# Optimization experiments

Measured on AMD Instinct MI355X. Metric: run time of the kernel, lower is better.

## Reference

```python
import jax, jax.numpy as jnp
import numpy as np

KH = KW = 5          # deformable kernel (matches offset_channels = 2*5*5)
PAD = 2              # (5-1)//2
DG = 4               # deformable groups


def conv3d(x, w, padding, bias=None):
    # x: [N,C,D,H,W], w: [O,I,kd,kh,kw]
    out = jax.lax.conv_general_dilated(
        x, w, window_strides=(1, 1, 1), padding=padding,
        dimension_numbers=('NCDHW', 'OIDHW', 'NCDHW'))
    if bias is not None:
        out = out + bias[None, :, None, None, None]
    return out


def deform_conv2d(x, offset, weight, pad=PAD, dg=DG):
    """torchvision/mmcv-style deformable conv, stride 1, groups=1, no bias.
    x: [N,C,H,W]; offset: [N, dg*2*K, H, W] ordered (group, k, (dy,dx));
    weight: [Cout, C, KH, KW]."""
    N, C, H, W = x.shape
    K = KH * KW
    off = offset.reshape(N, dg, K, 2, H, W)
    ky, kx = jnp.meshgrid(jnp.arange(KH), jnp.arange(KW), indexing='ij')
    ky = ky.reshape(K).astype(x.dtype)
    kx = kx.reshape(K).astype(x.dtype)
    # absolute sampling positions: [N,dg,K,H,W]
    base_y = ky[:, None, None] - pad + jnp.arange(H, dtype=x.dtype)[None, :, None]
    base_x = kx[:, None, None] - pad + jnp.arange(W, dtype=x.dtype)[None, None, :]
    sy = base_y[None, None] + off[:, :, :, 0]
    sx = base_x[None, None] + off[:, :, :, 1]
    y0 = jnp.floor(sy)
    x0 = jnp.floor(sx)
    wy = sy - y0
    wx = sx - x0
    y0i = y0.astype(jnp.int32)
    x0i = x0.astype(jnp.int32)
    Cg = C // dg
    xg = x.reshape(N, dg, Cg, H * W)

    def gather(yi, xi):
        valid = (yi >= 0) & (yi < H) & (xi >= 0) & (xi < W)
        yc = jnp.clip(yi, 0, H - 1)
        xc = jnp.clip(xi, 0, W - 1)
        idx = (yc * W + xc).reshape(N, dg, 1, K * H * W)
        v = jnp.take_along_axis(xg, idx, axis=3).reshape(N, dg, Cg, K, H, W)
        return v * valid[:, :, None].astype(x.dtype)

    v00 = gather(y0i, x0i)
    v01 = gather(y0i, x0i + 1)
    v10 = gather(y0i + 1, x0i)
    v11 = gather(y0i + 1, x0i + 1)
    wy_ = wy[:, :, None]
    wx_ = wx[:, :, None]
    samp = (v00 * (1 - wy_) * (1 - wx_) + v01 * (1 - wy_) * wx_
            + v10 * wy_ * (1 - wx_) + v11 * wy_ * wx_)
    samp = samp.reshape(N, C, K, H, W)             # deform groups only affect offsets
    wmat = weight.reshape(weight.shape[0], C, K)
    return jnp.einsum('nckhw,ock->nohw', samp, wmat)


def setup_inputs() -> dict:
    key = jax.random.key(0)
    k0, k1, k2, k3, k4 = jax.random.split(key, 5)
    bs, C, T, H, W = 1, 256, 4, 48, 48
    x = jax.random.normal(k0, (bs, C, T, H, W), dtype=jnp.float32)
    # spatio_offset: Conv3d(C -> dg*2*K, kernel (1,5,5), pad (0,2,2), no bias)
    w_off = jax.random.normal(k1, (DG * 2 * KH * KW, C, 1, KH, KW), dtype=jnp.float32) * 0.01
    # spatio_adaption: DeformConv2d weight, init std=0.01 (per init_weights)
    w_def = jax.random.normal(k2, (C, C, KH, KW), dtype=jnp.float32) * 0.01
    # temporal: Conv3d(C -> C, kernel (3,3,3), pad (1,1,1), with bias)
    fan_in = C * 27
    w_temp = jax.random.normal(k3, (C, C, 3, 3, 3), dtype=jnp.float32) * (1.0 / np.sqrt(fan_in))
    b_temp = jax.random.normal(k4, (C,), dtype=jnp.float32) * 0.01
    return {'x': x, 'w_off': w_off, 'w_def': w_def, 'w_temp': w_temp, 'b_temp': b_temp}


def reference(x, w_off, w_def, w_temp, b_temp):
    bs, C, T, H, W = x.shape
    # offset branch uses detached input (torch: x.detach())
    offset = conv3d(jax.lax.stop_gradient(x), w_off, [(0, 0), (PAD, PAD), (PAD, PAD)])
    off_fold = offset.transpose(0, 2, 1, 3, 4).reshape(bs * T, -1, H, W)
    x_fold = x.transpose(0, 2, 1, 3, 4).reshape(bs * T, C, H, W)
    x_spatio_fold = deform_conv2d(x_fold, off_fold, w_def)
    x_spatio = x_spatio_fold.reshape(bs, T, C, H, W).transpose(0, 2, 1, 3, 4)
    # cascaded=False branch: temporal conv on original x, then residual sum
    x_temporal = conv3d(x, w_temp, [(1, 1), (1, 1), (1, 1)], b_temp)
    return x_spatio + x_temporal
```

## Files before the change

kernel.cpp:

```cpp
#include <hip/hip_runtime.h>
#include <hip/hip_bf16.h>

#define T    4
#define C    256
#define H    48
#define W    48
#define HW   2304
#define OFFC 200
#define CK5  6400
#define CK9  2304
#define NFULL 9216
#define BPAD 72

typedef __attribute__((ext_vector_type(8))) short bf16x8;
typedef __attribute__((ext_vector_type(4))) float f32x4;

__device__ __forceinline__ unsigned short f2bf(float f) {
    unsigned int u = __float_as_uint(f);
    return (unsigned short)((u + 0x7FFFu + ((u >> 16) & 1u)) >> 16);
}
__device__ __forceinline__ float bflo(unsigned int v) { return __uint_as_float(v << 16); }
__device__ __forceinline__ float bfhi(unsigned int v) { return __uint_as_float(v & 0xFFFF0000u); }
__device__ __forceinline__ unsigned int pack2(float lo, float hi) {
    __hip_bfloat162 h = __float22bfloat162_rn(make_float2(lo, hi));
    return *reinterpret_cast<unsigned int*>(&h);
}
__device__ __forceinline__ void gload16(const void* g, void* l) {
    __builtin_amdgcn_global_load_lds(
        (const __attribute__((address_space(1))) unsigned int*)g,
        (__attribute__((address_space(3))) unsigned int*)l, 16, 0, 0);
}

__global__ __launch_bounds__(256) void prep_xt_k(const float* __restrict__ x,
                                                 const float* __restrict__ w_off,
                                                 const float* __restrict__ w_def,
                                                 const float* __restrict__ w_temp,
                                                 const float* __restrict__ bias,
                                                 unsigned short* __restrict__ wbo,
                                                 unsigned short* __restrict__ wbd,
                                                 unsigned short* __restrict__ wbT,
                                                 float* __restrict__ offb,
                                                 float* __restrict__ out,
                                                 unsigned short* __restrict__ xt) {
    __shared__ float tile[64][65];
    if (blockIdx.x >= 24320) {
        const int zb = blockIdx.x - 24320;
        const int p0 = (zb % 36) * 64, c0 = ((zb / 36) & 3) * 64, t = zb / 144;
        const int px = threadIdx.x & 63, sub = threadIdx.x >> 6;
        for (int cl = sub; cl < 64; cl += 4)
            tile[px][cl] = x[((long)(c0 + cl) * T + t) * HW + p0 + px];
        __syncthreads();
        const int seg = sub * 16;
        unsigned int pk[8];
        #pragma unroll
        for (int d = 0; d < 8; ++d)
            pk[d] = pack2(tile[px][seg + d * 2], tile[px][seg + d * 2 + 1]);
        unsigned short* orow = xt + ((long)t * HW + p0 + px) * 256 + c0 + seg;
        *(uint4*)(orow + 0) = make_uint4(pk[0], pk[1], pk[2], pk[3]);
        *(uint4*)(orow + 8) = make_uint4(pk[4], pk[5], pk[6], pk[7]);
        return;
    }
    long i = (long)blockIdx.x * 256 + threadIdx.x;
    if (i < 1638400) {
        const int c = (int)(i & 255); const int rest = (int)(i >> 8);
        const int q = rest % 25, o = rest / 25;
        wbo[(long)o * CK5 + q * 256 + c] =
            (o < OFFC) ? f2bf(w_off[((long)o * 256 + c) * 25 + q]) : (unsigned short)0;
    } else if (i < 3276800) {
        i -= 1638400;
        const int c = (int)(i & 255); const int rest = (int)(i >> 8);
        const int q = rest % 25, o = rest / 25;
        wbd[(long)o * CK5 + q * 256 + c] = f2bf(w_def[((long)o * 256 + c) * 25 + q]);
    } else if (i < 5046272) {
        i -= 3276800;
        const int c = (int)(i & 255); const int rest = (int)(i >> 8);
        const int j = rest % 9, oo = rest / 9;
        const int o = oo & 255, kt = oo >> 8;
        wbT[(long)kt * (256 * CK9) + (long)o * CK9 + j * 256 + c] =
            f2bf(w_temp[((long)o * 256 + c) * 27 + kt * 9 + j]);
    } else if (i < 5636096) {
        i -= 5046272;
        ((float4*)offb)[i] = make_float4(0.f, 0.f, 0.f, 0.f);
    } else {
        i -= 5636096;
        const float b = bias[(int)(i / 2304)];
        ((float4*)out)[i] = make_float4(b, b, b, b);
    }
}

__device__ __forceinline__ void mfma_iter(const unsigned short* __restrict__ Asl,
                                          const unsigned short* __restrict__ Bsl,
                                          int wave, int quad, int l16, f32x4 acc[4][2]) {
    const int wm = (wave & 1) * 64, wn = (wave >> 1) * 32;
    #pragma unroll
    for (int kh = 0; kh < 2; ++kh) {
        bf16x8 af[4], bfr[2];
        #pragma unroll
        for (int i = 0; i < 4; ++i) {
            const int row = wm + i * 16 + l16;
            const int slot = (kh * 4 + quad + (l16 & 7)) & 7;
            af[i] = *(const bf16x8*)(Asl + row * 64 + slot * 8);
        }
        #pragma unroll
        for (int j = 0; j < 2; ++j)
            bfr[j] = *(const bf16x8*)(Bsl + (wn + j * 16 + l16) * BPAD + kh * 32 + quad * 8);
        #pragma unroll
        for (int i = 0; i < 4; ++i)
            #pragma unroll
            for (int j = 0; j < 2; ++j)
                acc[i][j] = __builtin_amdgcn_mfma_f32_16x16x32_bf16(af[i], bfr[j], acc[i][j], 0, 0, 0);
    }
}
__device__ __forceinline__ void epilogue_atomic(float* __restrict__ Cf, int m0, int n0,
                                                int wave, int quad, int l16,
                                                int Mvalid, f32x4 acc[4][2]) {
    const int wm = (wave & 1) * 64, wn = (wave >> 1) * 32;
    #pragma unroll
    for (int i = 0; i < 4; ++i)
        #pragma unroll
        for (int rr = 0; rr < 4; ++rr) {
            const int o = m0 + wm + i * 16 + quad * 4 + rr;
            if (o >= Mvalid) continue;
            #pragma unroll
            for (int j = 0; j < 2; ++j)
                unsafeAtomicAdd(Cf + (long)o * NFULL + n0 + wn + j * 16 + l16, acc[i][j][rr]);
        }
}

__global__ __launch_bounds__(256, 4) void gemm_off_k(const unsigned short* __restrict__ A,
                                                     const unsigned short* __restrict__ xt,
                                                     float* __restrict__ Cf) {
    __shared__ unsigned short Asl[128 * 64];
    __shared__ unsigned short Bsl[128 * BPAD];
    const int tid = threadIdx.x;
    const int wave = tid >> 6, lane = tid & 63;
    const int quad = lane >> 4, l16 = lane & 15;
    const int n0 = blockIdx.x * 128, m0 = blockIdx.y * 128, k0 = blockIdx.z * 1280;
    const int t = n0 / HW, p0 = n0 - t * HW;
    const int wm = (wave & 1) * 64, wn = (wave >> 1) * 64;

    const int r8 = lane >> 3, s8 = lane & 7;
    const int qg = (s8 - r8) & 7;
    const long ldAb = (long)CK5 * 2;
    const char* Ap = (const char*)A + (long)(m0 + wave * 32 + r8) * ldAb
                     + (long)k0 * 2 + qg * 16;
    const long rstep8 = 8 * ldAb;
    unsigned short* la = Asl + wave * 2048;

    const int px = tid >> 1, half = tid & 1;
    const int p = p0 + px, h = p / 48, w = p - h * 48;
    const unsigned short* xts = xt + (long)t * HW * 256 + half * 32;

    auto produce = [&](int kk, uint4 v[4]) {
        const int q = kk >> 8, cb = kk & 255;
        const int d = q / 5;
        const int y = h + d - 2, xx = w + (q - d * 5) - 2;
        v[0] = make_uint4(0u, 0u, 0u, 0u); v[1] = v[0]; v[2] = v[0]; v[3] = v[0];
        if ((y >= 0) & (y < 48) & (xx >= 0) & (xx < 48)) {
            const unsigned short* bp = xts + (y * 48 + xx) * 256 + cb;
            #pragma unroll
            for (int d4 = 0; d4 < 4; ++d4) v[d4] = *(const uint4*)(bp + d4 * 8);
        }
    };

    uint4 cv[4];
    produce(k0, cv);

    f32x4 acc[4][4] = {};
    for (int i = 0; i < 20; ++i) {
        __syncthreads();
        #pragma unroll
        for (int c2 = 0; c2 < 4; ++c2) gload16(Ap + c2 * rstep8, la + c2 * 512);
        Ap += 128;
        #pragma unroll
        for (int d4 = 0; d4 < 4; ++d4)
            *(uint4*)(Bsl + px * BPAD + half * 32 + d4 * 8) = cv[d4];
        __syncthreads();
        if (i + 1 < 20) produce(k0 + (i + 1) * 64, cv);
        #pragma unroll
        for (int kh = 0; kh < 2; ++kh) {
            bf16x8 af[4], bfr[4];
            #pragma unroll
            for (int ii = 0; ii < 4; ++ii) {
                const int row = wm + ii * 16 + l16;
                const int slot = (kh * 4 + quad + (l16 & 7)) & 7;
                af[ii] = *(const bf16x8*)(Asl + row * 64 + slot * 8);
            }
            #pragma unroll
            for (int j = 0; j < 4; ++j)
                bfr[j] = *(const bf16x8*)(Bsl + (wn + j * 16 + l16) * BPAD + kh * 32 + quad * 8);
            #pragma unroll
            for (int ii = 0; ii < 4; ++ii)
                #pragma unroll
                for (int j = 0; j < 4; ++j)
                    acc[ii][j] = __builtin_amdgcn_mfma_f32_16x16x32_bf16(af[ii], bfr[j], acc[ii][j], 0, 0, 0);
        }
    }
    #pragma unroll
    for (int i = 0; i < 4; ++i)
        #pragma unroll
        for (int rr = 0; rr < 4; ++rr) {
            const int o = m0 + wm + i * 16 + quad * 4 + rr;
            if (o >= OFFC) continue;
            #pragma unroll
            for (int j = 0; j < 4; ++j)
                unsafeAtomicAdd(Cf + (long)o * NFULL + n0 + wn + j * 16 + l16, acc[i][j][rr]);
        }
}

__device__ __forceinline__ void pos_calc(int h, int w, int q, float dy, float dx,
                                         float wgt[4], int idx[4]) {
    const int d = q / 5;
    const int qy = d - 2, qx = q - d * 5 - 2;
    const float sy = (float)(h + qy) + dy;
    const float sx = (float)(w + qx) + dx;
    const float y0f = floorf(sy), x0f = floorf(sx);
    const float wy = sy - y0f, wx = sx - x0f;
    const int y0 = (int)y0f, x0 = (int)x0f;
    const int y1 = y0 + 1, x1 = x0 + 1;
    float w00 = (1.f - wy) * (1.f - wx);
    float w01 = (1.f - wy) * wx;
    float w10 = wy * (1.f - wx);
    float w11 = wy * wx;
    const bool vy0 = (y0 >= 0) & (y0 < 48), vy1 = (y1 >= 0) & (y1 < 48);
    const bool vx0 = (x0 >= 0) & (x0 < 48), vx1 = (x1 >= 0) & (x1 < 48);
    if (!(vy0 & vx0)) w00 = 0.f;
    if (!(vy0 & vx1)) w01 = 0.f;
    if (!(vy1 & vx0)) w10 = 0.f;
    if (!(vy1 & vx1)) w11 = 0.f;
    const int yc0 = min(max(y0, 0), 47), yc1 = min(max(y1, 0), 47);
    const int xc0 = min(max(x0, 0), 47), xc1 = min(max(x1, 0), 47);
    wgt[0] = w00; wgt[1] = w01; wgt[2] = w10; wgt[3] = w11;
    idx[0] = yc0 * 48 + xc0; idx[1] = yc0 * 48 + xc1;
    idx[2] = yc1 * 48 + xc0; idx[3] = yc1 * 48 + xc1;
}
__device__ __forceinline__ uint4 blend4(const uint4 u[4], const float wgt[4]) {
    unsigned int pk[4];
    #pragma unroll
    for (int qi = 0; qi < 4; ++qi) {
        const unsigned int a = ((const unsigned int*)&u[0])[qi];
        const unsigned int b = ((const unsigned int*)&u[1])[qi];
        const unsigned int c = ((const unsigned int*)&u[2])[qi];
        const unsigned int d = ((const unsigned int*)&u[3])[qi];
        const float rl = wgt[0] * bflo(a) + wgt[1] * bflo(b) + wgt[2] * bflo(c) + wgt[3] * bflo(d);
        const float rh = wgt[0] * bfhi(a) + wgt[1] * bfhi(b) + wgt[2] * bfhi(c) + wgt[3] * bfhi(d);
        pk[qi] = pack2(rl, rh);
    }
    return make_uint4(pk[0], pk[1], pk[2], pk[3]);
}

__device__ __forceinline__ void gemm_def_body(unsigned short* __restrict__ Asl,
                                              unsigned short* __restrict__ Bsl,
                                              const unsigned short* __restrict__ A,
                                              const unsigned short* __restrict__ xt,
                                              const float* __restrict__ offb,
                                              float* __restrict__ Cf,
                                              int m0, int n0, int k0) {
    const int tid = threadIdx.x;
    const int wave = tid >> 6, lane = tid & 63;
    const int quad = lane >> 4, l16 = lane & 15;
    const int t = n0 / HW, p0 = n0 - t * HW;
    const int px = tid >> 2, seg = tid & 3;
    const int p = p0 + px, h = p / 48, w = p - h * 48;
    const int nabs = n0 + px;
    const unsigned short* xts = xt + (long)t * HW * 256 + seg * 8;

    const int r8 = lane >> 3, s8 = lane & 7;
    const int qg = (s8 - r8) & 7;
    const long ldAb = (long)CK5 * 2;
    const char* Ap = (const char*)A + (long)(m0 + wave * 32 + r8) * ldAb
                     + (long)k0 * 2 + qg * 16;
    const long rstep8 = 8 * ldAb;
    unsigned short* la = Asl + wave * 2048;

    auto off_load = [&](int kk, float& dy, float& dx) {
        const int q = kk >> 8, g = (kk & 255) >> 6;
        dy = offb[(long)(g * 50 + 2 * q) * NFULL + nabs];
        dx = offb[(long)(g * 50 + 2 * q + 1) * NFULL + nabs];
    };
    auto corners = [&](int kk, float dy, float dx, uint4 u[8], float wgt[4]) {
        const int cb = kk & 255;
        int idx[4];
        pos_calc(h, w, kk >> 8, dy, dx, wgt, idx);
        #pragma unroll
        for (int cn = 0; cn < 4; ++cn) {
            const unsigned short* bp = xts + idx[cn] * 256 + cb;
            u[cn]     = *(const uint4*)bp;
            u[cn + 4] = *(const uint4*)(bp + 32);
        }
    };

    uint4 pkv0, pkv1;
    float dyN, dxN;
    {
        float dy0, dx0;
        off_load(k0, dy0, dx0);
        uint4 u[8]; float wg[4];
        corners(k0, dy0, dx0, u, wg);
        pkv0 = blend4(u, wg);
        pkv1 = blend4(u + 4, wg);
        off_load(k0 + 64, dyN, dxN);
    }

    f32x4 acc[4][2] = {};
    for (int i = 0; i < 25; ++i) {
        const int kk = k0 + i * 64;
        __syncthreads();
        #pragma unroll
        for (int c2 = 0; c2 < 4; ++c2) gload16(Ap + c2 * rstep8, la + c2 * 512);
        Ap += 128;
        *(uint4*)(Bsl + px * BPAD + seg * 8)      = pkv0;
        *(uint4*)(Bsl + px * BPAD + 32 + seg * 8) = pkv1;
        __syncthreads();
        const bool more = (i + 1 < 25);
        uint4 u[8]; float wg[4];
        if (more) {
            corners(kk + 64, dyN, dxN, u, wg);
            if (i + 2 < 25) off_load(kk + 128, dyN, dxN);
        }
        mfma_iter(Asl, Bsl, wave, quad, l16, acc);
        if (more) {
            pkv0 = blend4(u, wg);
            pkv1 = blend4(u + 4, wg);
        }
    }
    epilogue_atomic(Cf, m0, n0, wave, quad, l16, C, acc);
}

__device__ __forceinline__ void gemm_temp_body(unsigned short* __restrict__ Asl,
                                               unsigned short* __restrict__ Bsl,
                                               const unsigned short* __restrict__ A,
                                               const unsigned short* __restrict__ xt, int tsrc,
                                               float* __restrict__ Cf,
                                               int m0, int n0, int k0) {
    const int tid = threadIdx.x;
    const int wave = tid >> 6, lane = tid & 63;
    const int quad = lane >> 4, l16 = lane & 15;
    const int t = n0 / HW, p0 = n0 - t * HW;
    const int px = tid >> 2, seg = tid & 3;
    const int p = p0 + px, h = p / 48, w = p - h * 48;
    const unsigned short* xts = xt + (long)tsrc * HW * 256 + seg * 8;

    const int r8 = lane >> 3, s8 = lane & 7;
    const int qg = (s8 - r8) & 7;
    const long ldAb = (long)CK9 * 2;
    const char* Ap = (const char*)A + (long)(m0 + wave * 32 + r8) * ldAb
                     + (long)k0 * 2 + qg * 16;
    const long rstep8 = 8 * ldAb;
    unsigned short* la = Asl + wave * 2048;

    auto produce = [&](int kk, uint4& v0, uint4& v1) {
        const int q = kk >> 8, cb = kk & 255;
        const int d = q / 3;
        const int y = h + d - 1, xx = w + (q - d * 3) - 1;
        v0 = make_uint4(0u, 0u, 0u, 0u); v1 = v0;
        if ((y >= 0) & (y < 48) & (xx >= 0) & (xx < 48)) {
            const unsigned short* bp = xts + (y * 48 + xx) * 256 + cb;
            v0 = *(const uint4*)bp; v1 = *(const uint4*)(bp + 32);
        }
    };

    uint4 cv0, cv1;
    produce(k0, cv0, cv1);

    f32x4 acc[4][2] = {};
    for (int i = 0; i < 18; ++i) {
        __syncthreads();
        #pragma unroll
        for (int c2 = 0; c2 < 4; ++c2) gload16(Ap + c2 * rstep8, la + c2 * 512);
        Ap += 128;
        *(uint4*)(Bsl + px * BPAD + seg * 8)      = cv0;
        *(uint4*)(Bsl + px * BPAD + 32 + seg * 8) = cv1;
        __syncthreads();
        if (i + 1 < 18) produce(k0 + (i + 1) * 64, cv0, cv1);
        mfma_iter(Asl, Bsl, wave, quad, l16, acc);
    }
    epilogue_atomic(Cf, m0, n0, wave, quad, l16, C, acc);
}

__global__ __launch_bounds__(256, 4) void gemm_dt_k(const unsigned short* __restrict__ wbd,
                                                    const unsigned short* __restrict__ wbT,
                                                    const unsigned short* __restrict__ xt,
                                                    const float* __restrict__ offb,
                                                    float* __restrict__ out) {
    __shared__ unsigned short Asl[128 * 64];
    __shared__ unsigned short Bsl[64 * BPAD];
    const int z = blockIdx.z, n0 = blockIdx.x * 64, m0 = blockIdx.y * 128;
    if (z < 4) {
        gemm_def_body(Asl, Bsl, wbd, xt, offb, out, m0, n0, z * 1600);
    } else {
        const int zz = z - 4, kt = zz >> 1, half = zz & 1;
        const int t = n0 / HW, tsrc = t + kt - 1;
        if (tsrc < 0 || tsrc >= T) return;
        gemm_temp_body(Asl, Bsl, wbT + (long)kt * 256 * CK9, xt, tsrc, out,
                       m0, n0, half * 1152);
    }
}

extern "C" void kernel_launch(void* const* d_in, const int* in_sizes, int n_in,
                              void* d_out, int out_size, void* d_ws, size_t ws_size,
                              hipStream_t stream) {
    const float* x      = (const float*)d_in[0];
    const float* w_off  = (const float*)d_in[1];
    const float* w_def  = (const float*)d_in[2];
    const float* w_temp = (const float*)d_in[3];
    const float* b_temp = (const float*)d_in[4];
    float* out = (float*)d_out;

    unsigned short* xt   = (unsigned short*)d_ws;
    float*          offb = (float*)((char*)d_ws + 4718592ul);
    unsigned short* wbo  = (unsigned short*)((char*)d_ws + 14155776ul);
    unsigned short* wbd  = (unsigned short*)((char*)d_ws + 17432576ul);
    unsigned short* wbT  = (unsigned short*)((char*)d_ws + 20709376ul);

    prep_xt_k<<<24896, 256, 0, stream>>>(x, w_off, w_def, w_temp, b_temp,
                                         wbo, wbd, wbT, offb, out, xt);
    gemm_off_k<<<dim3(72, 2, 5), 256, 0, stream>>>(wbo, xt, offb);
    gemm_dt_k<<<dim3(144, 2, 10), 256, 0, stream>>>(wbd, wbT, xt, offb, out);
}
```

Measured before the change: 289.3 us.

## Double K-tile depth to 128 in deform/temporal GEMMs and rebalance split-K

The fused deformable and temporal GEMM kernel now stages 128-wide K tiles instead of 64, using a new swizzled A-staging helper and a wider padded B tile. This halves the number of barrier-separated iterations, and each thread gathers and blends 32 channels per bilinear sample instead of 16. Split-K is rebalanced: the deform part goes from 4 to 5 chunks, the temporal part drops its 2-way K split, and the offset GEMM goes from 5 to 10 K-splits. The larger shared-memory footprint forces launch bounds down to 3 blocks per SM. Per-thread register pressure for the 16 corner vectors also rises.

```diff
diff --git a/kernel.cpp b/kernel.cpp
--- a/kernel.cpp
+++ b/kernel.cpp
@@ -10,7 +10,8 @@
 #define CK5  6400
 #define CK9  2304
 #define NFULL 9216
-#define BPAD 72
+#define BPAD64  72
+#define BPAD128 136
 
 typedef __attribute__((ext_vector_type(8))) short bf16x8;
 typedef __attribute__((ext_vector_type(4))) float f32x4;
@@ -88,54 +89,15 @@
     }
 }
 
-__device__ __forceinline__ void mfma_iter(const unsigned short* __restrict__ Asl,
-                                          const unsigned short* __restrict__ Bsl,
-                                          int wave, int quad, int l16, f32x4 acc[4][2]) {
-    const int wm = (wave & 1) * 64, wn = (wave >> 1) * 32;
-    #pragma unroll
-    for (int kh = 0; kh < 2; ++kh) {
-        bf16x8 af[4], bfr[2];
-        #pragma unroll
-        for (int i = 0; i < 4; ++i) {
-            const int row = wm + i * 16 + l16;
-            const int slot = (kh * 4 + quad + (l16 & 7)) & 7;
-            af[i] = *(const bf16x8*)(Asl + row * 64 + slot * 8);
-        }
-        #pragma unroll
-        for (int j = 0; j < 2; ++j)
-            bfr[j] = *(const bf16x8*)(Bsl + (wn + j * 16 + l16) * BPAD + kh * 32 + quad * 8);
-        #pragma unroll
-        for (int i = 0; i < 4; ++i)
-            #pragma unroll
-            for (int j = 0; j < 2; ++j)
-                acc[i][j] = __builtin_amdgcn_mfma_f32_16x16x32_bf16(af[i], bfr[j], acc[i][j], 0, 0, 0);
-    }
-}
-__device__ __forceinline__ void epilogue_atomic(float* __restrict__ Cf, int m0, int n0,
-                                                int wave, int quad, int l16,
-                                                int Mvalid, f32x4 acc[4][2]) {
-    const int wm = (wave & 1) * 64, wn = (wave >> 1) * 32;
-    #pragma unroll
-    for (int i = 0; i < 4; ++i)
-        #pragma unroll
-        for (int rr = 0; rr < 4; ++rr) {
-            const int o = m0 + wm + i * 16 + quad * 4 + rr;
-            if (o >= Mvalid) continue;
-            #pragma unroll
-            for (int j = 0; j < 2; ++j)
-                unsafeAtomicAdd(Cf + (long)o * NFULL + n0 + wn + j * 16 + l16, acc[i][j][rr]);
-        }
-}
-
 __global__ __launch_bounds__(256, 4) void gemm_off_k(const unsigned short* __restrict__ A,
                                                      const unsigned short* __restrict__ xt,
                                                      float* __restrict__ Cf) {
     __shared__ unsigned short Asl[128 * 64];
-    __shared__ unsigned short Bsl[128 * BPAD];
+    __shared__ unsigned short Bsl[128 * BPAD64];
     const int tid = threadIdx.x;
     const int wave = tid >> 6, lane = tid & 63;
     const int quad = lane >> 4, l16 = lane & 15;
-    const int n0 = blockIdx.x * 128, m0 = blockIdx.y * 128, k0 = blockIdx.z * 1280;
+    const int n0 = blockIdx.x * 128, m0 = blockIdx.y * 128, k0 = blockIdx.z * 640;
     const int t = n0 / HW, p0 = n0 - t * HW;
     const int wm = (wave & 1) * 64, wn = (wave >> 1) * 64;
 
@@ -167,16 +129,16 @@
     produce(k0, cv);
 
     f32x4 acc[4][4] = {};
-    for (int i = 0; i < 20; ++i) {
+    for (int i = 0; i < 10; ++i) {
         __syncthreads();
         #pragma unroll
         for (int c2 = 0; c2 < 4; ++c2) gload16(Ap + c2 * rstep8, la + c2 * 512);
         Ap += 128;
         #pragma unroll
         for (int d4 = 0; d4 < 4; ++d4)
-            *(uint4*)(Bsl + px * BPAD + half * 32 + d4 * 8) = cv[d4];
-        __syncthreads();
-        if (i + 1 < 20) produce(k0 + (i + 1) * 64, cv);
+            *(uint4*)(Bsl + px * BPAD64 + half * 32 + d4 * 8) = cv[d4];
+        __syncthreads();
+        if (i + 1 < 10) produce(k0 + (i + 1) * 64, cv);
         #pragma unroll
         for (int kh = 0; kh < 2; ++kh) {
             bf16x8 af[4], bfr[4];
@@ -188,7 +150,7 @@
             }
             #pragma unroll
             for (int j = 0; j < 4; ++j)
-                bfr[j] = *(const bf16x8*)(Bsl + (wn + j * 16 + l16) * BPAD + kh * 32 + quad * 8);
+                bfr[j] = *(const bf16x8*)(Bsl + (wn + j * 16 + l16) * BPAD64 + kh * 32 + quad * 8);
             #pragma unroll
             for (int ii = 0; ii < 4; ++ii)
                 #pragma unroll
@@ -206,6 +168,76 @@
             for (int j = 0; j < 4; ++j)
                 unsafeAtomicAdd(Cf + (long)o * NFULL + n0 + wn + j * 16 + l16, acc[i][j][rr]);
         }
+}
+
+__device__ __forceinline__ void mfma_iter128(const unsigned short* __restrict__ Asl,
+                                             const unsigned short* __restrict__ Bsl,
+                                             int wave, int quad, int l16, f32x4 acc[4][2]) {
+    const int wm = (wave & 1) * 64, wn = (wave >> 1) * 32;
+    #pragma unroll
+    for (int kh = 0; kh < 4; ++kh) {
+        const int kc = kh * 4 + quad;
+        bf16x8 af[4], bfr[2];
+        #pragma unroll
+        for (int i = 0; i < 4; ++i) {
+            const int row = wm + i * 16 + l16;
+            const int slot = (((kc & 7) + (l16 & 7)) & 7) | (kc & 8);
+            af[i] = *(const bf16x8*)(Asl + row * 128 + slot * 8);
+        }
+        #pragma unroll
+        for (int j = 0; j < 2; ++j)
+            bfr[j] = *(const bf16x8*)(Bsl + (wn + j * 16 + l16) * BPAD128 + kh * 32 + quad * 8);
+        #pragma unroll
+        for (int i = 0; i < 4; ++i)
+            #pragma unroll
+            for (int j = 0; j < 2; ++j)
+                acc[i][j] = __builtin_amdgcn_mfma_f32_16x16x32_bf16(af[i], bfr[j], acc[i][j], 0, 0, 0);
+    }
+}
+__device__ __forceinline__ void epilogue_atomic(float* __restrict__ Cf, int m0, int n0,
+                                                int wave, int quad, int l16,
+                                                int Mvalid, f32x4 acc[4][2]) {
+    const int wm = (wave & 1) * 64, wn = (wave >> 1) * 32;
+    #pragma unroll
+    for (int i = 0; i < 4; ++i)
+        #pragma unroll
+        for (int rr = 0; rr < 4; ++rr) {
+            const int o = m0 + wm + i * 16 + quad * 4 + rr;
+            if (o >= Mvalid) continue;
+            #pragma unroll
+            for (int j = 0; j < 2; ++j)
+                unsafeAtomicAdd(Cf + (long)o * NFULL + n0 + wn + j * 16 + l16, acc[i][j][rr]);
+        }
+}
+
+struct AStage128 {
+    const char* Ap0;
+    const char* Ap1;
+    long rstep;
+    unsigned short* la;
+};
+__device__ __forceinline__ AStage128 astage_init(const unsigned short* A, long ldA,
+                                                 int m0, int k0, int wave, int lane,
+                                                 unsigned short* Asl) {
+    const int r4 = lane >> 4, s8 = lane & 7, hi8 = lane & 8;
+    const int row0 = r4, row1 = 4 + r4;
+    const int g0 = ((s8 - row0) & 7) | hi8;
+    const int g1 = ((s8 - row1) & 7) | hi8;
+    AStage128 st;
+    const long ldAb = ldA * 2;
+    st.Ap0 = (const char*)A + (long)(m0 + wave * 32 + row0) * ldAb + (long)k0 * 2 + g0 * 16;
+    st.Ap1 = (const char*)A + (long)(m0 + wave * 32 + row1) * ldAb + (long)k0 * 2 + g1 * 16;
+    st.rstep = 8 * ldAb;
+    st.la = Asl + wave * 32 * 128;
+    return st;
+}
+__device__ __forceinline__ void astage_issue(AStage128& st) {
+    #pragma unroll
+    for (int pr = 0; pr < 4; ++pr) {
+        gload16(st.Ap0 + pr * st.rstep, st.la + (2 * pr) * 512);
+        gload16(st.Ap1 + pr * st.rstep, st.la + (2 * pr + 1) * 512);
+    }
+    st.Ap0 += 256; st.Ap1 += 256;
 }
 
 __device__ __forceinline__ void pos_calc(int h, int w, int q, float dy, float dx,
@@ -234,14 +266,16 @@
     idx[0] = yc0 * 48 + xc0; idx[1] = yc0 * 48 + xc1;
     idx[2] = yc1 * 48 + xc0; idx[3] = yc1 * 48 + xc1;
 }
-__device__ __forceinline__ uint4 blend4(const uint4 u[4], const float wgt[4]) {
+__device__ __forceinline__ uint4 blend1(const uint4& ua, const uint4& ub,
+                                        const uint4& uc, const uint4& ud,
+                                        const float wgt[4]) {
     unsigned int pk[4];
     #pragma unroll
     for (int qi = 0; qi < 4; ++qi) {
-        const unsigned int a = ((const unsigned int*)&u[0])[qi];
-        const unsigned int b = ((const unsigned int*)&u[1])[qi];
-        const unsigned int c = ((const unsigned int*)&u[2])[qi];
-        const unsigned int d = ((const unsigned int*)&u[3])[qi];
+        const unsigned int a = ((const unsigned int*)&ua)[qi];
+        const unsigned int b = ((const unsigned int*)&ub)[qi];
+        const unsigned int c = ((const unsigned int*)&uc)[qi];
+        const unsigned int d = ((const unsigned int*)&ud)[qi];
         const float rl = wgt[0] * bflo(a) + wgt[1] * bflo(b) + wgt[2] * bflo(c) + wgt[3] * bflo(d);
         const float rh = wgt[0] * bfhi(a) + wgt[1] * bfhi(b) + wgt[2] * bfhi(c) + wgt[3] * bfhi(d);
         pk[qi] = pack2(rl, rh);
@@ -263,66 +297,61 @@
     const int px = tid >> 2, seg = tid & 3;
     const int p = p0 + px, h = p / 48, w = p - h * 48;
     const int nabs = n0 + px;
-    const unsigned short* xts = xt + (long)t * HW * 256 + seg * 8;
-
-    const int r8 = lane >> 3, s8 = lane & 7;
-    const int qg = (s8 - r8) & 7;
-    const long ldAb = (long)CK5 * 2;
-    const char* Ap = (const char*)A + (long)(m0 + wave * 32 + r8) * ldAb
-                     + (long)k0 * 2 + qg * 16;
-    const long rstep8 = 8 * ldAb;
-    unsigned short* la = Asl + wave * 2048;
+    const unsigned short* xts = xt + (long)t * HW * 256 + seg * 32;
+
+    AStage128 st = astage_init(A, CK5, m0, k0, wave, lane, Asl);
 
     auto off_load = [&](int kk, float& dy, float& dx) {
-        const int q = kk >> 8, g = (kk & 255) >> 6;
+        const int q = kk >> 8;
+        const int g = ((kk & 255) >> 6) + (seg >> 1);
         dy = offb[(long)(g * 50 + 2 * q) * NFULL + nabs];
         dx = offb[(long)(g * 50 + 2 * q + 1) * NFULL + nabs];
     };
-    auto corners = [&](int kk, float dy, float dx, uint4 u[8], float wgt[4]) {
+    auto corners = [&](int kk, float dy, float dx, uint4 u[16], float wgt[4]) {
         const int cb = kk & 255;
         int idx[4];
         pos_calc(h, w, kk >> 8, dy, dx, wgt, idx);
         #pragma unroll
         for (int cn = 0; cn < 4; ++cn) {
             const unsigned short* bp = xts + idx[cn] * 256 + cb;
-            u[cn]     = *(const uint4*)bp;
-            u[cn + 4] = *(const uint4*)(bp + 32);
+            #pragma unroll
+            for (int d4 = 0; d4 < 4; ++d4) u[cn * 4 + d4] = *(const uint4*)(bp + d4 * 8);
         }
     };
-
-    uint4 pkv0, pkv1;
+    auto blend_all = [&](const uint4 u[16], const float wg[4], uint4 pk[4]) {
+        #pragma unroll
+        for (int d4 = 0; d4 < 4; ++d4)
+            pk[d4] = blend1(u[d4], u[4 + d4], u[8 + d4], u[12 + d4], wg);
+    };
+
+    uint4 pk[4];
     float dyN, dxN;
     {
         float dy0, dx0;
         off_load(k0, dy0, dx0);
-        uint4 u[8]; float wg[4];
+        uint4 u[16]; float wg[4];
         corners(k0, dy0, dx0, u, wg);
-        pkv0 = blend4(u, wg);
-        pkv1 = blend4(u + 4, wg);
-        off_load(k0 + 64, dyN, dxN);
+        blend_all(u, wg, pk);
+        off_load(k0 + 128, dyN, dxN);
     }
 
     f32x4 acc[4][2] = {};
-    for (int i = 0; i < 25; ++i) {
-        const int kk = k0 + i * 64;
-        __syncthreads();
-        #pragma unroll
-        for (int c2 = 0; c2 < 4; ++c2) gload16(Ap + c2 * rstep8, la + c2 * 512);
-        Ap += 128;
-        *(uint4*)(Bsl + px * BPAD + seg * 8)      = pkv0;
-        *(uint4*)(Bsl + px * BPAD + 32 + seg * 8) = pkv1;
-        __syncthreads();
-        const bool more = (i + 1 < 25);
-        uint4 u[8]; float wg[4];
+    for (int i = 0; i < 10; ++i) {
+        const int kk = k0 + i * 128;
+        __syncthreads();
+        astage_issue(st);
+        #pragma unroll
+        for (int d4 = 0; d4 < 4; ++d4)
+            *(uint4*)(Bsl + px * BPAD128 + seg * 32 + d4 * 8) = pk[d4];
+        __syncthreads();
+        const bool more = (i + 1 < 10);
+        uint4 u[16]; float wg[4];
         if (more) {
-            corners(kk + 64, dyN, dxN, u, wg);
-            if (i + 2 < 25) off_load(kk + 128, dyN, dxN);
-        }
-        mfma_iter(Asl, Bsl, wave, quad, l16, acc);
-        if (more) {
-            pkv0 = blend4(u, wg);
-            pkv1 = blend4(u + 4, wg);
-        }
+            corners(kk + 128, dyN, dxN, u, wg);
+            if (i + 2 < 10) off_load(kk + 256, dyN, dxN);
+        }
+        mfma_iter128(Asl, Bsl, wave, quad, l16, acc);
+        if (more) blend_all(u, wg, pk);
     }
     epilogue_atomic(Cf, m0, n0, wave, quad, l16, C, acc);
 }
@@ -332,68 +361,61 @@
                                                const unsigned short* __restrict__ A,
                                                const unsigned short* __restrict__ xt, int tsrc,
                                                float* __restrict__ Cf,
-                                               int m0, int n0, int k0) {
+                                               int m0, int n0) {
     const int tid = threadIdx.x;
     const int wave = tid >> 6, lane = tid & 63;
     const int quad = lane >> 4, l16 = lane & 15;
     const int t = n0 / HW, p0 = n0 - t * HW;
     const int px = tid >> 2, seg = tid & 3;
     const int p = p0 + px, h = p / 48, w = p - h * 48;
-    const unsigned short* xts = xt + (long)tsrc * HW * 256 + seg * 8;
-
-    const int r8 = lane >> 3, s8 = lane & 7;
-    const int qg = (s8 - r8) & 7;
-    const long ldAb = (long)CK9 * 2;
-    const char* Ap = (const char*)A + (long)(m0 + wave * 32 + r8) * ldAb
-                     + (long)k0 * 2 + qg * 16;
-    const long rstep8 = 8 * ldAb;
-    unsigned short* la = Asl + wave * 2048;
-
-    auto produce = [&](int kk, uint4& v0, uint4& v1) {
+    const unsigned short* xts = xt + (long)tsrc * HW * 256 + seg * 32;
+
+    AStage128 st = astage_init(A, CK9, m0, 0, wave, lane, Asl);
+
+    auto produce = [&](int kk, uint4 v[4]) {
         const int q = kk >> 8, cb = kk & 255;
         const int d = q / 3;
         const int y = h + d - 1, xx = w + (q - d * 3) - 1;
-        v0 = make_uint4(0u, 0u, 0u, 0u); v1 = v0;
+        v[0] = make_uint4(0u, 0u, 0u, 0u); v[1] = v[0]; v[2] = v[0]; v[3] = v[0];
         if ((y >= 0) & (y < 48) & (xx >= 0) & (xx < 48)) {
             const unsigned short* bp = xts + (y * 48 + xx) * 256 + cb;
-            v0 = *(const uint4*)bp; v1 = *(const uint4*)(bp + 32);
+            #pragma unroll
+            for (int d4 = 0; d4 < 4; ++d4) v[d4] = *(const uint4*)(bp + d4 * 8);
         }
     };
 
-    uint4 cv0, cv1;
-    produce(k0, cv0, cv1);
+    uint4 cv[4];
+    produce(0, cv);
 
     f32x4 acc[4][2] = {};
     for (int i = 0; i < 18; ++i) {
         __syncthreads();
-        #pragma unroll
-        for (int c2 = 0; c2 < 4; ++c2) gload16(Ap + c2 * rstep8, la + c2 * 512);
-        Ap += 128;
-        *(uint4*)(Bsl + px * BPAD + seg * 8)      = cv0;
-        *(uint4*)(Bsl + px * BPAD + 32 + seg * 8) = cv1;
-        __syncthreads();
-        if (i + 1 < 18) produce(k0 + (i + 1) * 64, cv0, cv1);
-        mfma_iter(Asl, Bsl, wave, quad, l16, acc);
+        astage_issue(st);
+        #pragma unroll
+        for (int d4 = 0; d4 < 4; ++d4)
+            *(uint4*)(Bsl + px * BPAD128 + seg * 32 + d4 * 8) = cv[d4];
+        __syncthreads();
+        if (i + 1 < 18) produce((i + 1) * 128, cv);
+        mfma_iter128(Asl, Bsl, wave, quad, l16, acc);
     }
     epilogue_atomic(Cf, m0, n0, wave, quad, l16, C, acc);
 }
 
-__global__ __launch_bounds__(256, 4) void gemm_dt_k(const unsigned short* __restrict__ wbd,
+__global__ __launch_bounds__(256, 3) void gemm_dt_k(const unsigned short* __restrict__ wbd,
                                                     const unsigned short* __restrict__ wbT,
                                                     const unsigned short* __restrict__ xt,
                                                     const float* __restrict__ offb,
                                                     float* __restrict__ out) {
-    __shared__ unsigned short Asl[128 * 64];
-    __shared__ unsigned short Bsl[64 * BPAD];
+    __shared__ unsigned short Asl[128 * 128];
+    __shared__ unsigned short Bsl[64 * BPAD128];
     const int z = blockIdx.z, n0 = blockIdx.x * 64, m0 = blockIdx.y * 128;
-    if (z < 4) {
-        gemm_def_body(Asl, Bsl, wbd, xt, offb, out, m0, n0, z * 1600);
+    if (z < 5) {
+        gemm_def_body(Asl, Bsl, wbd, xt, offb, out, m0, n0, z * 1280);
     } else {
-        const int zz = z - 4, kt = zz >> 1, half = zz & 1;
+        const int kt = z - 5;
         const int t = n0 / HW, tsrc = t + kt - 1;
         if (tsrc < 0 || tsrc >= T) return;
-        gemm_temp_body(Asl, Bsl, wbT + (long)kt * 256 * CK9, xt, tsrc, out,
-                       m0, n0, half * 1152);
+        gemm_temp_body(Asl, Bsl, wbT + (long)kt * 256 * CK9, xt, tsrc, out, m0, n0);
     }
 }
 
@@ -415,6 +437,6 @@
 
     prep_xt_k<<<24896, 256, 0, stream>>>(x, w_off, w_def, w_temp, b_temp,
                                          wbo, wbd, wbT, offb, out, xt);
-    gemm_off_k<<<dim3(72, 2, 5), 256, 0, stream>>>(wbo, xt, offb);
-    gemm_dt_k<<<dim3(144, 2, 10), 256, 0, stream>>>(wbd, wbT, xt, offb, out);
-}
+    gemm_off_k<<<dim3(72, 2, 10), 256, 0, stream>>>(wbo, xt, offb);
+    gemm_dt_k<<<dim3(144, 2, 8), 256, 0, stream>>>(wbd, wbT, xt, offb, out);
+}
```

Measured after the change: 329.6 us. 1.14x slower.

## Rebalance split-K across offset, deformable and temporal GEMMs; widen temporal N tile

Applied to the files above, without the earlier changes.

The offset GEMM now uses twice as many K splits (10 instead of 5), and the deformable GEMM moves from 4 to 5 splits, giving more blocks per launch. The temporal conv body switches to a 128-wide N tile with a 4x4 accumulator per wave, reusing the wider MFMA helper, and the shared B buffer grows to match. The aim is better load balance and occupancy across the fused launch, and more reuse of each A tile in the temporal part. The cost is more atomic-add traffic into the outputs, larger shared memory and register use per block, and idle blocks in the temporal grid.

```diff
diff --git a/kernel.cpp b/kernel.cpp
--- a/kernel.cpp
+++ b/kernel.cpp
@@ -88,33 +88,33 @@
     }
 }
 
-__device__ __forceinline__ void mfma_iter(const unsigned short* __restrict__ Asl,
-                                          const unsigned short* __restrict__ Bsl,
-                                          int wave, int quad, int l16, f32x4 acc[4][2]) {
-    const int wm = (wave & 1) * 64, wn = (wave >> 1) * 32;
+__device__ __forceinline__ void mfma_iter_w(const unsigned short* __restrict__ Asl,
+                                            const unsigned short* __restrict__ Bsl,
+                                            int wave, int quad, int l16, f32x4 acc[4][4]) {
+    const int wm = (wave & 1) * 64, wn = (wave >> 1) * 64;
     #pragma unroll
     for (int kh = 0; kh < 2; ++kh) {
-        bf16x8 af[4], bfr[2];
-        #pragma unroll
-        for (int i = 0; i < 4; ++i) {
-            const int row = wm + i * 16 + l16;
+        bf16x8 af[4], bfr[4];
+        #pragma unroll
+        for (int ii = 0; ii < 4; ++ii) {
+            const int row = wm + ii * 16 + l16;
             const int slot = (kh * 4 + quad + (l16 & 7)) & 7;
-            af[i] = *(const bf16x8*)(Asl + row * 64 + slot * 8);
-        }
-        #pragma unroll
-        for (int j = 0; j < 2; ++j)
+            af[ii] = *(const bf16x8*)(Asl + row * 64 + slot * 8);
+        }
+        #pragma unroll
+        for (int j = 0; j < 4; ++j)
             bfr[j] = *(const bf16x8*)(Bsl + (wn + j * 16 + l16) * BPAD + kh * 32 + quad * 8);
         #pragma unroll
-        for (int i = 0; i < 4; ++i)
-            #pragma unroll
-            for (int j = 0; j < 2; ++j)
-                acc[i][j] = __builtin_amdgcn_mfma_f32_16x16x32_bf16(af[i], bfr[j], acc[i][j], 0, 0, 0);
-    }
-}
-__device__ __forceinline__ void epilogue_atomic(float* __restrict__ Cf, int m0, int n0,
-                                                int wave, int quad, int l16,
-                                                int Mvalid, f32x4 acc[4][2]) {
-    const int wm = (wave & 1) * 64, wn = (wave >> 1) * 32;
+        for (int ii = 0; ii < 4; ++ii)
+            #pragma unroll
+            for (int j = 0; j < 4; ++j)
+                acc[ii][j] = __builtin_amdgcn_mfma_f32_16x16x32_bf16(af[ii], bfr[j], acc[ii][j], 0, 0, 0);
+    }
+}
+__device__ __forceinline__ void epilogue_atomic_w(float* __restrict__ Cf, int m0, int n0,
+                                                  int wave, int quad, int l16,
+                                                  int Mvalid, f32x4 acc[4][4]) {
+    const int wm = (wave & 1) * 64, wn = (wave >> 1) * 64;
     #pragma unroll
     for (int i = 0; i < 4; ++i)
         #pragma unroll
@@ -122,7 +122,7 @@
             const int o = m0 + wm + i * 16 + quad * 4 + rr;
             if (o >= Mvalid) continue;
             #pragma unroll
-            for (int j = 0; j < 2; ++j)
+            for (int j = 0; j < 4; ++j)
                 unsafeAtomicAdd(Cf + (long)o * NFULL + n0 + wn + j * 16 + l16, acc[i][j][rr]);
         }
 }
@@ -135,9 +135,8 @@
     const int tid = threadIdx.x;
     const int wave = tid >> 6, lane = tid & 63;
     const int quad = lane >> 4, l16 = lane & 15;
-    const int n0 = blockIdx.x * 128, m0 = blockIdx.y * 128, k0 = blockIdx.z * 1280;
+    const int n0 = blockIdx.x * 128, m0 = blockIdx.y * 128, k0 = blockIdx.z * 640;
     const int t = n0 / HW, p0 = n0 - t * HW;
-    const int wm = (wave & 1) * 64, wn = (wave >> 1) * 64;
 
     const int r8 = lane >> 3, s8 = lane & 7;
     const int qg = (s8 - r8) & 7;
@@ -167,7 +166,7 @@
     produce(k0, cv);
 
     f32x4 acc[4][4] = {};
-    for (int i = 0; i < 20; ++i) {
+    for (int i = 0; i < 10; ++i) {
         __syncthreads();
         #pragma unroll
         for (int c2 = 0; c2 < 4; ++c2) gload16(Ap + c2 * rstep8, la + c2 * 512);
@@ -176,34 +175,47 @@
         for (int d4 = 0; d4 < 4; ++d4)
             *(uint4*)(Bsl + px * BPAD + half * 32 + d4 * 8) = cv[d4];
         __syncthreads();
-        if (i + 1 < 20) produce(k0 + (i + 1) * 64, cv);
-        #pragma unroll
-        for (int kh = 0; kh < 2; ++kh) {
-            bf16x8 af[4], bfr[4];
-            #pragma unroll
-            for (int ii = 0; ii < 4; ++ii) {
-                const int row = wm + ii * 16 + l16;
-                const int slot = (kh * 4 + quad + (l16 & 7)) & 7;
-                af[ii] = *(const bf16x8*)(Asl + row * 64 + slot * 8);
-            }
-            #pragma unroll
-            for (int j = 0; j < 4; ++j)
-                bfr[j] = *(const bf16x8*)(Bsl + (wn + j * 16 + l16) * BPAD + kh * 32 + quad * 8);
-            #pragma unroll
-            for (int ii = 0; ii < 4; ++ii)
-                #pragma unroll
-                for (int j = 0; j < 4; ++j)
-                    acc[ii][j] = __builtin_amdgcn_mfma_f32_16x16x32_bf16(af[ii], bfr[j], acc[ii][j], 0, 0, 0);
-        }
-    }
+        if (i + 1 < 10) produce(k0 + (i + 1) * 64, cv);
+        mfma_iter_w(Asl, Bsl, wave, quad, l16, acc);
+    }
+    epilogue_atomic_w(Cf, m0, n0, wave, quad, l16, OFFC, acc);
+}
+
+__device__ __forceinline__ void mfma_iter(const unsigned short* __restrict__ Asl,
+                                          const unsigned short* __restrict__ Bsl,
+                                          int wave, int quad, int l16, f32x4 acc[4][2]) {
+    const int wm = (wave & 1) * 64, wn = (wave >> 1) * 32;
+    #pragma unroll
+    for (int kh = 0; kh < 2; ++kh) {
+        bf16x8 af[4], bfr[2];
+        #pragma unroll
+        for (int i = 0; i < 4; ++i) {
+            const int row = wm + i * 16 + l16;
+            const int slot = (kh * 4 + quad + (l16 & 7)) & 7;
+            af[i] = *(const bf16x8*)(Asl + row * 64 + slot * 8);
+        }
+        #pragma unroll
+        for (int j = 0; j < 2; ++j)
+            bfr[j] = *(const bf16x8*)(Bsl + (wn + j * 16 + l16) * BPAD + kh * 32 + quad * 8);
+        #pragma unroll
+        for (int i = 0; i < 4; ++i)
+            #pragma unroll
+            for (int j = 0; j < 2; ++j)
+                acc[i][j] = __builtin_amdgcn_mfma_f32_16x16x32_bf16(af[i], bfr[j], acc[i][j], 0, 0, 0);
+    }
+}
+__device__ __forceinline__ void epilogue_atomic(float* __restrict__ Cf, int m0, int n0,
+                                                int wave, int quad, int l16,
+                                                int Mvalid, f32x4 acc[4][2]) {
+    const int wm = (wave & 1) * 64, wn = (wave >> 1) * 32;
     #pragma unroll
     for (int i = 0; i < 4; ++i)
         #pragma unroll
         for (int rr = 0; rr < 4; ++rr) {
             const int o = m0 + wm + i * 16 + quad * 4 + rr;
-            if (o >= OFFC) continue;
-            #pragma unroll
-            for (int j = 0; j < 4; ++j)
+            if (o >= Mvalid) continue;
+            #pragma unroll
+            for (int j = 0; j < 2; ++j)
                 unsafeAtomicAdd(Cf + (long)o * NFULL + n0 + wn + j * 16 + l16, acc[i][j][rr]);
         }
 }
@@ -303,7 +315,7 @@
     }
 
     f32x4 acc[4][2] = {};
-    for (int i = 0; i < 25; ++i) {
+    for (int i = 0; i < 20; ++i) {
         const int kk = k0 + i * 64;
         __syncthreads();
         #pragma unroll
@@ -312,11 +324,11 @@
         *(uint4*)(Bsl + px * BPAD + seg * 8)      = pkv0;
         *(uint4*)(Bsl + px * BPAD + 32 + seg * 8) = pkv1;
         __syncthreads();
-        const bool more = (i + 1 < 25);
+        const bool more = (i + 1 < 20);
         uint4 u[8]; float wg[4];
         if (more) {
             corners(kk + 64, dyN, dxN, u, wg);
-            if (i + 2 < 25) off_load(kk + 128, dyN, dxN);
+            if (i + 2 < 20) off_load(kk + 128, dyN, dxN);
         }
         mfma_iter(Asl, Bsl, wave, quad, l16, acc);
         if (more) {
@@ -337,9 +349,9 @@
     const int wave = tid >> 6, lane = tid & 63;
     const int quad = lane >> 4, l16 = lane & 15;
     const int t = n0 / HW, p0 = n0 - t * HW;
-    const int px = tid >> 2, seg = tid & 3;
+    const int px = tid >> 1, half = tid & 1;
     const int p = p0 + px, h = p / 48, w = p - h * 48;
-    const unsigned short* xts = xt + (long)tsrc * HW * 256 + seg * 8;
+    const unsigned short* xts = xt + (long)tsrc * HW * 256 + half * 32;
 
     const int r8 = lane >> 3, s8 = lane & 7;
     const int qg = (s8 - r8) & 7;
@@ -349,33 +361,35 @@
     const long rstep8 = 8 * ldAb;
     unsigned short* la = Asl + wave * 2048;
 
-    auto produce = [&](int kk, uint4& v0, uint4& v1) {
+    auto produce = [&](int kk, uint4 v[4]) {
         const int q = kk >> 8, cb = kk & 255;
         const int d = q / 3;
         const int y = h + d - 1, xx = w + (q - d * 3) - 1;
-        v0 = make_uint4(0u, 0u, 0u, 0u); v1 = v0;
+        v[0] = make_uint4(0u, 0u, 0u, 0u); v[1] = v[0]; v[2] = v[0]; v[3] = v[0];
         if ((y >= 0) & (y < 48) & (xx >= 0) & (xx < 48)) {
             const unsigned short* bp = xts + (y * 48 + xx) * 256 + cb;
-            v0 = *(const uint4*)bp; v1 = *(const uint4*)(bp + 32);
+            #pragma unroll
+            for (int d4 = 0; d4 < 4; ++d4) v[d4] = *(const uint4*)(bp + d4 * 8);
         }
     };
 
-    uint4 cv0, cv1;
-    produce(k0, cv0, cv1);
-
-    f32x4 acc[4][2] = {};
+    uint4 cv[4];
+    produce(k0, cv);
+
+    f32x4 acc[4][4] = {};
     for (int i = 0; i < 18; ++i) {
         __syncthreads();
         #pragma unroll
         for (int c2 = 0; c2 < 4; ++c2) gload16(Ap + c2 * rstep8, la + c2 * 512);
         Ap += 128;
-        *(uint4*)(Bsl + px * BPAD + seg * 8)      = cv0;
-        *(uint4*)(Bsl + px * BPAD + 32 + seg * 8) = cv1;
-        __syncthreads();
-        if (i + 1 < 18) produce(k0 + (i + 1) * 64, cv0, cv1);
-        mfma_iter(Asl, Bsl, wave, quad, l16, acc);
-    }
-    epilogue_atomic(Cf, m0, n0, wave, quad, l16, C, acc);
+        #pragma unroll
+        for (int d4 = 0; d4 < 4; ++d4)
+            *(uint4*)(Bsl + px * BPAD + half * 32 + d4 * 8) = cv[d4];
+        __syncthreads();
+        if (i + 1 < 18) produce(k0 + (i + 1) * 64, cv);
+        mfma_iter_w(Asl, Bsl, wave, quad, l16, acc);
+    }
+    epilogue_atomic_w(Cf, m0, n0, wave, quad, l16, C, acc);
 }
 
 __global__ __launch_bounds__(256, 4) void gemm_dt_k(const unsigned short* __restrict__ wbd,
@@ -384,12 +398,15 @@
                                                     const float* __restrict__ offb,
                                                     float* __restrict__ out) {
     __shared__ unsigned short Asl[128 * 64];
-    __shared__ unsigned short Bsl[64 * BPAD];
-    const int z = blockIdx.z, n0 = blockIdx.x * 64, m0 = blockIdx.y * 128;
-    if (z < 4) {
-        gemm_def_body(Asl, Bsl, wbd, xt, offb, out, m0, n0, z * 1600);
+    __shared__ unsigned short Bsl[128 * BPAD];
+    const int z = blockIdx.z, m0 = blockIdx.y * 128;
+    if (z < 5) {
+        const int n0 = blockIdx.x * 64;
+        gemm_def_body(Asl, Bsl, wbd, xt, offb, out, m0, n0, z * 1280);
     } else {
-        const int zz = z - 4, kt = zz >> 1, half = zz & 1;
+        if (blockIdx.x >= 72) return;
+        const int n0 = blockIdx.x * 128;
+        const int zz = z - 5, kt = zz >> 1, half = zz & 1;
         const int t = n0 / HW, tsrc = t + kt - 1;
         if (tsrc < 0 || tsrc >= T) return;
         gemm_temp_body(Asl, Bsl, wbT + (long)kt * 256 * CK9, xt, tsrc, out,
@@ -415,6 +432,6 @@
 
     prep_xt_k<<<24896, 256, 0, stream>>>(x, w_off, w_def, w_temp, b_temp,
                                          wbo, wbd, wbT, offb, out, xt);
-    gemm_off_k<<<dim3(72, 2, 5), 256, 0, stream>>>(wbo, xt, offb);
-    gemm_dt_k<<<dim3(144, 2, 10), 256, 0, stream>>>(wbd, wbT, xt, offb, out);
-}
+    gemm_off_k<<<dim3(72, 2, 10), 256, 0, stream>>>(wbo, xt, offb);
+    gemm_dt_k<<<dim3(144, 2, 11), 256, 0, stream>>>(wbd, wbT, xt, offb, out);
+}
```

Measured after the change: 318.0 us. 9.9% more time.
